# Kernel optimization log

Hardware: AMD Instinct MI355X
Metric: run time of the kernel (lower is better)

The kernel has to match this reference:

```python
import jax, jax.numpy as jnp
import numpy as np
from jax import lax

DEPTH, HEADS, DH, DIM, M, V, NUM_EMB, D_VQ = 6, 8, 64, 512, 256, 523, 512, 64


def _ln(x, g, b):
    mu = jnp.mean(x, -1, keepdims=True)
    var = jnp.var(x, -1, keepdims=True)
    return (x - mu) * lax.rsqrt(var + 1e-5) * g + b


def _softmax_kernel(data, proj, is_query):
    # FAVOR+ positive softmax features (performer-pytorch softmax_kernel)
    dn = data * (data.shape[-1] ** -0.25)
    dd = jnp.einsum('bhld,md->bhlm', dn, proj)
    diag = 0.5 * jnp.sum(dn * dn, axis=-1, keepdims=True)
    mx = jnp.max(dd, axis=-1, keepdims=True) if is_query else jnp.max(dd)
    return jnp.exp(dd - diag - lax.stop_gradient(mx)) * (proj.shape[0] ** -0.5) + 1e-4


def _causal_linear_attn(qp, kp, v):
    # out_t = qp_t . cumsum_t(kp v^T) / (qp_t . cumsum_t(kp))
    kc = jnp.cumsum(kp, axis=2)
    den = jnp.einsum('bhlm,bhlm->bhl', qp, kc)
    kv = jnp.cumsum(jnp.einsum('bhlm,bhld->bhlmd', kp, v), axis=2)
    return jnp.einsum('bhlm,bhlmd->bhld', qp, kv) / den[..., None]


def _vq_encode(_x, conv1_w, conv1_b, conv2_w, conv2_b, codebook):
    dn = ('NCDHW', 'OIDHW', 'NCDHW')
    h = lax.conv_general_dilated(_x, conv1_w, (2, 2, 2), [(1, 1)] * 3, dimension_numbers=dn)
    h = jax.nn.relu(h + conv1_b[None, :, None, None, None])
    h = lax.conv_general_dilated(h, conv2_w, (2, 2, 2), [(1, 1)] * 3, dimension_numbers=dn)
    h = h + conv2_b[None, :, None, None, None]                 # [N, D, 4,4,4]
    z = jnp.transpose(h, (0, 2, 3, 4, 1))                      # [N, 4,4,4, D]
    flat = z.reshape(-1, z.shape[-1])
    d2 = (jnp.sum(flat * flat, 1, keepdims=True)
          - 2.0 * flat @ codebook.T
          + jnp.sum(codebook * codebook, 1)[None, :])
    inds = jnp.argmin(d2, axis=1).astype(jnp.int32)
    return inds.reshape(z.shape[:4])                           # [N, 4,4,4]


def _performer_loss(seq, tok_emb, pos_emb, proj, ln1_g, ln1_b, wq, wk, wv, wo, bo,
                    ln2_g, ln2_b, ff1_w, ff1_b, ff2_w, ff2_b, lnf_g, lnf_b,
                    logits_w, logits_b):
    inp, tgt = seq[:, :-1], seq[:, 1:]
    b, L = inp.shape
    h = tok_emb[inp] + pos_emb[:L][None]
    split = lambda t: jnp.transpose(t.reshape(b, L, HEADS, DH), (0, 2, 1, 3))
    for l in range(DEPTH):
        x1 = _ln(h, ln1_g[l], ln1_b[l])
        q, k, v = split(x1 @ wq[l]), split(x1 @ wk[l]), split(x1 @ wv[l])
        qp = _softmax_kernel(q, proj[l], True)
        kp = _softmax_kernel(k, proj[l], False)
        o = _causal_linear_attn(qp, kp, v)
        o = jnp.transpose(o, (0, 2, 1, 3)).reshape(b, L, DIM)
        h = h + o @ wo[l] + bo[l]
        x2 = _ln(h, ln2_g[l], ln2_b[l])
        h = h + jax.nn.gelu(x2 @ ff1_w[l] + ff1_b[l]) @ ff2_w[l] + ff2_b[l]
    h = _ln(h, lnf_g, lnf_b)
    logits = h @ logits_w + logits_b
    lp = jax.nn.log_softmax(logits, axis=-1)
    nll = -jnp.take_along_axis(lp, tgt[..., None], axis=-1)[..., 0]
    return jnp.mean(nll)


def setup_inputs() -> dict:
    key = jax.random.key(0)
    ks = jax.random.split(key, 24)
    n = lambda k, sh, s=0.02: (jax.random.normal(k, sh) * s).astype(jnp.float32)
    bs = 16
    return {
        'x': jax.random.normal(ks[0], (bs, 1, 16, 16, 16), jnp.float32),
        'xn': jax.random.normal(ks[1], (bs, 1, 1, 16, 16, 16), jnp.float32),
        'i': jax.random.randint(ks[2], (bs, 3), 0, V, jnp.int32),
        # frozen VQ-VAE
        'conv1_w': n(ks[3], (32, 1, 4, 4, 4), 0.1), 'conv1_b': jnp.zeros((32,), jnp.float32),
        'conv2_w': n(ks[4], (D_VQ, 32, 4, 4, 4), 0.05), 'conv2_b': jnp.zeros((D_VQ,), jnp.float32),
        'codebook': jax.random.normal(ks[5], (NUM_EMB, D_VQ), jnp.float32),
        # FAVOR+ random-feature projections (non-trainable buffer)
        'proj': jax.random.normal(ks[6], (DEPTH, M, DH), jnp.float32),
        # performer params
        'tok_emb': n(ks[7], (V, DIM)), 'pos_emb': n(ks[8], (131, DIM)),
        'ln1_g': jnp.ones((DEPTH, DIM), jnp.float32), 'ln1_b': jnp.zeros((DEPTH, DIM), jnp.float32),
        'wq': n(ks[9], (DEPTH, DIM, DIM)), 'wk': n(ks[10], (DEPTH, DIM, DIM)),
        'wv': n(ks[11], (DEPTH, DIM, DIM)), 'wo': n(ks[12], (DEPTH, DIM, DIM)),
        'bo': jnp.zeros((DEPTH, DIM), jnp.float32),
        'ln2_g': jnp.ones((DEPTH, DIM), jnp.float32), 'ln2_b': jnp.zeros((DEPTH, DIM), jnp.float32),
        'ff1_w': n(ks[13], (DEPTH, DIM, 4 * DIM)), 'ff1_b': jnp.zeros((DEPTH, 4 * DIM), jnp.float32),
        'ff2_w': n(ks[14], (DEPTH, 4 * DIM, DIM)), 'ff2_b': jnp.zeros((DEPTH, DIM), jnp.float32),
        'lnf_g': jnp.ones((DIM,), jnp.float32), 'lnf_b': jnp.zeros((DIM,), jnp.float32),
        'logits_w': n(ks[15], (DIM, V)), 'logits_b': jnp.zeros((V,), jnp.float32),
    }


def reference(x, xn, i, conv1_w, conv1_b, conv2_w, conv2_b, codebook, proj,
              tok_emb, pos_emb, ln1_g, ln1_b, wq, wk, wv, wo, bo, ln2_g, ln2_b,
              ff1_w, ff1_b, ff2_w, ff2_b, lnf_g, lnf_b, logits_w, logits_b):
    bs = x.shape[0]
    _xn = xn.reshape((-1,) + xn.shape[2:])            # (b n) c x y z
    _x = jnp.concatenate([x, _xn], axis=0)
    inds = _vq_encode(_x, conv1_w, conv1_b, conv2_w, conv2_b, codebook)
    inds_i = inds[:bs].reshape(bs, -1)                # b (x y z)
    inds_r = inds[bs:].reshape(bs, -1)                # b (n x y z)
    seq = jnp.concatenate([i.astype(jnp.int32), inds_r, inds_i], axis=1)  # [b, 131]
    return _performer_loss(seq, tok_emb, pos_emb, proj, ln1_g, ln1_b, wq, wk, wv, wo,
                           bo, ln2_g, ln2_b, ff1_w, ff1_b, ff2_w, ff2_b,
                           lnf_g, lnf_b, logits_w, logits_b)
```

## Files before the change

### kernel.cpp

```cpp
#include <hip/hip_runtime.h>

#define SEQL 130
#define LSEQ 131
#define DIMM 512
#define NHEADS 8
#define MF 256
#define VSZ 523
#define NROWS (16*SEQL)
#define NBH (16*NHEADS)
#define NBHL (NBH*SEQL)
#define QSEG 1064960

typedef __attribute__((ext_vector_type(8))) short short8;
typedef __attribute__((ext_vector_type(8))) unsigned short us8;
typedef __attribute__((ext_vector_type(4))) unsigned short us4;
typedef __attribute__((ext_vector_type(4))) float f32x4;

__device__ __forceinline__ unsigned short f2bf(float f){
  unsigned int u = __float_as_uint(f);
  u += 0x7fffu + ((u>>16)&1u);
  return (unsigned short)(u>>16);
}
__device__ __forceinline__ float bf2f(unsigned short h){
  return __uint_as_float(((unsigned int)h)<<16);
}
__device__ __forceinline__ float gelu_f(float x){
  float x3 = x*x*x;
  return 0.5f*x*(1.f+tanhf(0.7978845608028654f*(x+0.044715f*x3)));
}
__device__ __forceinline__ unsigned enc_max(float f){
  unsigned u = __float_as_uint(f);
  return (u & 0x80000000u) ? ~u : (u | 0x80000000u);
}
__device__ __forceinline__ float dec_max(unsigned k){
  unsigned u = (k>>31) ? (k & 0x7fffffffu) : ~k;
  return __uint_as_float(u);
}
__device__ __forceinline__ float blk_sum(float v){
  #pragma unroll
  for(int off=32;off;off>>=1) v += __shfl_xor(v,off);
  __shared__ float tmp_s[4];
  int t=threadIdx.x;
  if((t&63)==0) tmp_s[t>>6]=v;
  __syncthreads();
  v = tmp_s[0]+tmp_s[1]+tmp_s[2]+tmp_s[3];
  __syncthreads();
  return v;
}
__device__ __forceinline__ float blk_max(float v){
  #pragma unroll
  for(int off=32;off;off>>=1) v = fmaxf(v,__shfl_xor(v,off));
  __shared__ float tmp_m[4];
  int t=threadIdx.x;
  if((t&63)==0) tmp_m[t>>6]=v;
  __syncthreads();
  v = fmaxf(fmaxf(tmp_m[0],tmp_m[1]),fmaxf(tmp_m[2],tmp_m[3]));
  __syncthreads();
  return v;
}

__global__ __launch_bounds__(256) void conv1_k(const float* __restrict__ x,
    const float* __restrict__ xn, const float* __restrict__ w,
    const float* __restrict__ bias, float* __restrict__ out){
  int idx = blockIdx.x*256 + threadIdx.x;
  if(idx >= 32*32*8*8*8) return;
  int ow = idx & 7, oh = (idx>>3)&7, od = (idx>>6)&7, oc = (idx>>9)&31, n = idx>>14;
  const float* xp = (n<16) ? (x + n*4096) : (xn + (n-16)*4096);
  const float* wp = w + oc*64;
  float acc = bias[oc];
  #pragma unroll
  for(int kd=0;kd<4;kd++){ int id = od*2-1+kd; if((unsigned)id>=16u) continue;
    #pragma unroll
    for(int kh=0;kh<4;kh++){ int ih = oh*2-1+kh; if((unsigned)ih>=16u) continue;
      #pragma unroll
      for(int kw=0;kw<4;kw++){ int iw = ow*2-1+kw; if((unsigned)iw>=16u) continue;
        acc += xp[(id*16+ih)*16+iw]*wp[(kd*4+kh)*4+kw];
      }}}
  out[idx] = fmaxf(acc,0.f);
}

__global__ __launch_bounds__(256) void conv2_k(const float* __restrict__ c1,
    const float* __restrict__ w, const float* __restrict__ bias,
    float* __restrict__ out){
  __shared__ float in_s[32][4][120];
  int od = blockIdx.x, n = blockIdx.y;
  int t = threadIdx.x;
  float4* zf = (float4*)&in_s[0][0][0];
  #pragma unroll
  for(int j=0;j<15;j++) zf[t + 256*j] = make_float4(0.f,0.f,0.f,0.f);
  __syncthreads();
  #pragma unroll
  for(int j=0;j<4;j++){
    int ridx = t + 256*j;
    int ic = ridx>>5, rem = ridx&31;
    int kd = rem>>3, ih = rem&7;
    int id = od*2 - 1 + kd;
    if((unsigned)id < 8u){
      const float* src = c1 + (size_t)(n*32+ic)*512 + id*64 + ih*8;
      float4 a = *(const float4*)src;
      float4 b = *(const float4*)(src+4);
      float* dst = &in_s[ic][kd][(ih+1)*12 + 1];
      dst[0]=a.x; dst[1]=a.y; dst[2]=a.z; dst[3]=a.w;
      dst[4]=b.x; dst[5]=b.y; dst[6]=b.z; dst[7]=b.w;
    }
  }
  __syncthreads();
  int oc = t>>2, oh = t&3;
  float acc0=bias[oc], acc1=acc0, acc2=acc0, acc3=acc0;
  for(int ic=0; ic<32; ic++){
    #pragma unroll
    for(int kd=0;kd<4;kd++){
      #pragma unroll
      for(int kh=0;kh<4;kh++){
        const float* rp = &in_s[ic][kd][(oh*2+kh)*12];
        f32x4 f0 = *(const f32x4*)rp;
        f32x4 f1 = *(const f32x4*)(rp+4);
        f32x4 f2 = *(const f32x4*)(rp+8);
        f32x4 wv = *(const f32x4*)(w + ((size_t)(oc*32+ic)*64 + (kd*4+kh)*4));
        float in0=f0[0],in1=f0[1],in2=f0[2],in3=f0[3];
        float in4=f1[0],in5=f1[1],in6=f1[2],in7=f1[3];
        float in8=f2[0],in9=f2[1];
        acc0 += wv[0]*in0 + wv[1]*in1 + wv[2]*in2 + wv[3]*in3;
        acc1 += wv[0]*in2 + wv[1]*in3 + wv[2]*in4 + wv[3]*in5;
        acc2 += wv[0]*in4 + wv[1]*in5 + wv[2]*in6 + wv[3]*in7;
        acc3 += wv[0]*in6 + wv[1]*in7 + wv[2]*in8 + wv[3]*in9;
      }
    }
  }
  float4 res = make_float4(acc0,acc1,acc2,acc3);
  *(float4*)(out + (size_t)(n*64+oc)*64 + od*16 + oh*4) = res;
}

__global__ __launch_bounds__(256) void vq_k(const float* __restrict__ c2,
    const float* __restrict__ cb, int* __restrict__ inds){
  int nf = blockIdx.x;
  int nb = nf>>6, sp = nf&63;
  __shared__ float z[64];
  int t = threadIdx.x;
  if(t<64) z[t] = c2[(nb*64+t)*64 + sp];
  __syncthreads();
  float best = 3.0e38f; int bi = 0;
  for(int j=t; j<512; j+=256){
    const float* cr = cb + j*64;
    float dot=0.f, nn=0.f;
    #pragma unroll 8
    for(int d=0;d<64;d++){ float cv=cr[d]; dot += z[d]*cv; nn += cv*cv; }
    float dist = nn - 2.f*dot;
    if(dist < best){ best=dist; bi=j; }
  }
  #pragma unroll
  for(int off=32;off;off>>=1){
    float ob = __shfl_down(best,off); int oi = __shfl_down(bi,off);
    if(ob<best || (ob==best && oi<bi)){ best=ob; bi=oi; }
  }
  __shared__ float rb[4]; __shared__ int ri[4];
  if((t&63)==0){ rb[t>>6]=best; ri[t>>6]=bi; }
  __syncthreads();
  if(t==0){
    for(int wv=1;wv<4;wv++){ if(rb[wv]<best || (rb[wv]==best && ri[wv]<bi)){ best=rb[wv]; bi=ri[wv]; } }
    inds[nf]=bi;
  }
}

__global__ void seq_k(const int* __restrict__ iarr, const int* __restrict__ inds,
                      int* __restrict__ seq){
  int idx = blockIdx.x*256 + threadIdx.x;
  if(idx >= 16*LSEQ) return;
  int b = idx/LSEQ, p = idx%LSEQ;
  int v;
  if(p<3)       v = iarr[b*3+p];
  else if(p<67) v = inds[(16+b)*64 + (p-3)];
  else          v = inds[b*64 + (p-67)];
  seq[idx] = v;
}

__global__ __launch_bounds__(256) void embed_k(const int* __restrict__ seq,
    const float* __restrict__ tok, const float* __restrict__ pos,
    float* __restrict__ h){
  int idx = blockIdx.x*256 + threadIdx.x;
  int c = idx & 511; int row = idx >> 9;
  int b = row/SEQL, l = row - b*SEQL;
  int tk = seq[b*LSEQ + l];
  h[idx] = tok[tk*DIMM + c] + pos[l*DIMM + c];
}

__global__ __launch_bounds__(256) void ln_k(const float* __restrict__ in,
    const float* __restrict__ g, const float* __restrict__ bb,
    unsigned short* __restrict__ out){
  int row = blockIdx.x; int t = threadIdx.x;
  const float* xr = in + (size_t)row*DIMM;
  float x0 = xr[t], x1 = xr[t+256];
  float s = x0+x1, ss = x0*x0 + x1*x1;
  #pragma unroll
  for(int off=32;off;off>>=1){ s += __shfl_xor(s,off); ss += __shfl_xor(ss,off); }
  __shared__ float bs[4], bss[4];
  if((t&63)==0){ bs[t>>6]=s; bss[t>>6]=ss; }
  __syncthreads();
  s = bs[0]+bs[1]+bs[2]+bs[3]; ss = bss[0]+bss[1]+bss[2]+bss[3];
  float mu = s*(1.f/512.f);
  float var = ss*(1.f/512.f) - mu*mu;
  float inv = rsqrtf(var + 1e-5f);
  out[(size_t)row*DIMM+t]     = f2bf((x0-mu)*inv*g[t]     + bb[t]);
  out[(size_t)row*DIMM+t+256] = f2bf((x1-mu)*inv*g[t+256] + bb[t+256]);
}

__global__ __launch_bounds__(256) void wprep_k(const float* __restrict__ wq_l,
    const float* __restrict__ wk_l, const float* __restrict__ wv_l,
    const float* __restrict__ wo_l, const float* __restrict__ ff1_l,
    const float* __restrict__ ff2_l,
    unsigned short* __restrict__ wqkvt, unsigned short* __restrict__ wot,
    unsigned short* __restrict__ ff1t, unsigned short* __restrict__ ff2t,
    unsigned int* __restrict__ gmaxbits){
  int bid = blockIdx.x;
  int t = threadIdx.x;
  if(bid==0 && t==0) gmaxbits[0] = 0u;
  const float* src; unsigned short* dst;
  int n0, k0, srcN, dstK;
  if(bid < 768){
    int nt = bid % 48, kt = bid / 48;
    n0 = nt*32; k0 = kt*32;
    int seg = n0 >> 9;
    src = (seg==0 ? wq_l : seg==1 ? wk_l : wv_l);
    dst = wqkvt; srcN = 512; dstK = 512;
    n0 &= 0x1ff; n0 |= (seg<<9);
  } else if(bid < 1024){
    int b2 = bid-768; int nt = b2 % 16, kt = b2 / 16;
    n0 = nt*32; k0 = kt*32; src = wo_l; dst = wot; srcN = 512; dstK = 512;
  } else if(bid < 2048){
    int b2 = bid-1024; int nt = b2 % 64, kt = b2 / 64;
    n0 = nt*32; k0 = kt*32; src = ff1_l; dst = ff1t; srcN = 2048; dstK = 512;
  } else {
    int b2 = bid-2048; int nt = b2 % 16, kt = b2 / 16;
    n0 = nt*32; k0 = kt*32; src = ff2_l; dst = ff2t; srcN = 512; dstK = 2048;
  }
  int srcCol0 = (bid < 768) ? (n0 & 0x1ff) : n0;
  __shared__ float tile[32][33];
  int c = t&31, r = t>>5;
  #pragma unroll
  for(int j=0;j<4;j++)
    tile[r+8*j][c] = src[(size_t)(k0+r+8*j)*srcN + srcCol0 + c];
  __syncthreads();
  #pragma unroll
  for(int j=0;j<4;j++){
    int n = n0 + r + 8*j;
    dst[(size_t)n*dstK + k0 + c] = f2bf(tile[c][r+8*j]);
  }
}

__global__ __launch_bounds__(256) void wconv_k(const float* __restrict__ W,
    unsigned short* __restrict__ dst, int K, int N){
  __shared__ float tile[32][33];
  int k0 = blockIdx.y*32, n0 = blockIdx.x*32;
  int t = threadIdx.x; int c = t&31, r = t>>5;
  #pragma unroll
  for(int j=0;j<4;j++){
    int n = n0+c;
    tile[r+8*j][c] = (n<N) ? W[(size_t)(k0+r+8*j)*N + n] : 0.f;
  }
  __syncthreads();
  #pragma unroll
  for(int j=0;j<4;j++){
    int n = n0 + r + 8*j;
    if(n<N) dst[(size_t)n*K + k0 + c] = f2bf(tile[c][r+8*j]);
  }
}

__global__ __launch_bounds__(256) void projcv_k(const float* __restrict__ proj,
    unsigned short* __restrict__ pb){
  int i = blockIdx.x*256 + threadIdx.x;
  if(i < 6*MF*64) pb[i] = f2bf(proj[i]);
}

template<int MODE>
__global__ __launch_bounds__(256) void mgemm_k(const unsigned short* __restrict__ A,
    const unsigned short* __restrict__ Bt, const float* __restrict__ bias,
    float* __restrict__ Cf, unsigned short* __restrict__ Cb,
    int M, int N, int K){
  __shared__ unsigned short As[4096];
  __shared__ unsigned short Bs[4096];
  int t = threadIdx.x;
  const int m0 = blockIdx.y*64, n0 = blockIdx.x*64;
  int w = t>>6, l = t&63;
  int wr = w>>1, wc = w&1;
  f32x4 acc[2][2] = {};
  int srow = t>>2, sp = (t&3)*2;
  int arow = m0 + srow, brow = n0 + srow;
  bool aok = arow < M, bok = brow < N;
  const us8* Ap = (const us8*)(A + (size_t)arow*K + sp*8);
  const us8* Bp = (const us8*)(Bt + (size_t)brow*K + sp*8);
  unsigned short* Aw0 = As + srow*64 + (((sp  )^(srow&7))<<3);
  unsigned short* Aw1 = As + srow*64 + (((sp+1)^(srow&7))<<3);
  unsigned short* Bw0 = Bs + srow*64 + (((sp  )^(srow&7))<<3);
  unsigned short* Bw1 = Bs + srow*64 + (((sp+1)^(srow&7))<<3);
  for(int k0=0; k0<K; k0+=64){
    us8 a0={}, a1={}, b0={}, b1={};
    if(aok){ a0 = Ap[0]; a1 = Ap[1]; }
    if(bok){ b0 = Bp[0]; b1 = Bp[1]; }
    Ap += 8; Bp += 8;
    __syncthreads();
    *(us8*)Aw0 = a0; *(us8*)Aw1 = a1;
    *(us8*)Bw0 = b0; *(us8*)Bw1 = b1;
    __syncthreads();
    #pragma unroll
    for(int kk=0;kk<2;kk++){
      short8 af[2], bf[2];
      #pragma unroll
      for(int m=0;m<2;m++){
        int row = wr*32 + m*16 + (l&15);
        int slot = kk*4 + (l>>4);
        af[m] = *(const short8*)(As + row*64 + ((slot^(row&7))<<3));
      }
      #pragma unroll
      for(int n=0;n<2;n++){
        int col = wc*32 + n*16 + (l&15);
        int slot = kk*4 + (l>>4);
        bf[n] = *(const short8*)(Bs + col*64 + ((slot^(col&7))<<3));
      }
      #pragma unroll
      for(int m=0;m<2;m++)
        #pragma unroll
        for(int n=0;n<2;n++)
          acc[m][n] = __builtin_amdgcn_mfma_f32_16x16x32_bf16(af[m], bf[n], acc[m][n], 0, 0, 0);
    }
  }
  #pragma unroll
  for(int m=0;m<2;m++){
    #pragma unroll
    for(int n=0;n<2;n++){
      int col = n0 + wc*32 + n*16 + (l&15);
      #pragma unroll
      for(int i=0;i<4;i++){
        int row = m0 + wr*32 + m*16 + (l>>4)*4 + i;
        if(row < M && col < N){
          float v = acc[m][n][i];
          if(MODE==0){
            if(bias) v += bias[col];
            Cf[(size_t)row*N+col] = v;
          } else if(MODE==1){
            v *= (col < 1024) ? 0.35355339059327378f : 1.0f;
            int seg = col>>9, d0 = col&511;
            int hh = d0>>6, d = d0&63;
            int bb = row/SEQL, ll = row - bb*SEQL;
            Cb[(size_t)seg*QSEG + (((size_t)(bb*NHEADS+hh))*SEQL + ll)*64 + d] = f2bf(v);
          } else if(MODE==3){
            v += bias[col];
            Cf[(size_t)row*N+col] += v;
          } else {
            v += bias[col];
            v = gelu_f(v);
            Cb[(size_t)row*N+col] = f2bf(v);
          }
        }
      }
    }
  }
}

__global__ __launch_bounds__(256) void featA_k(const unsigned short* __restrict__ qn,
    const unsigned short* __restrict__ kn, const unsigned short* __restrict__ projl,
    unsigned short* __restrict__ qp, unsigned int* __restrict__ gmaxbits){
  int z = blockIdx.y;
  const unsigned short* dn = z ? kn : qn;
  __shared__ float uni[32*264];
  __shared__ unsigned short dns[2048];
  unsigned short* ps = (unsigned short*)uni;
  int t = threadIdx.x;
  size_t R0 = (size_t)blockIdx.x*32;
  {
    int row = t>>3, sl = t&7;
    us8 u = *(const us8*)(dn + (R0+row)*64 + sl*8);
    *(us8*)(dns + row*64 + ((sl^(row&7))<<3)) = u;
  }
  #pragma unroll
  for(int j=0;j<8;j++){
    int ridx = t + 256*j;
    int row = ridx>>3, sl = ridx&7;
    us8 u = *(const us8*)(projl + row*64 + sl*8);
    *(us8*)(ps + row*64 + ((sl^(row&7))<<3)) = u;
  }
  __syncthreads();
  int w = t>>6, l = t&63;
  int rt = w&1, cb = (w>>1)*8;
  f32x4 acc[8] = {};
  #pragma unroll
  for(int kk=0;kk<2;kk++){
    int ar = rt*16 + (l&15);
    int slot = kk*4 + (l>>4);
    short8 a = *(const short8*)(dns + ar*64 + ((slot^(ar&7))<<3));
    #pragma unroll
    for(int ct=0;ct<8;ct++){
      int br = (cb+ct)*16 + (l&15);
      short8 b = *(const short8*)(ps + br*64 + ((slot^(br&7))<<3));
      acc[ct] = __builtin_amdgcn_mfma_f32_16x16x32_bf16(a, b, acc[ct], 0, 0, 0);
    }
  }
  __syncthreads();
  #pragma unroll
  for(int ct=0;ct<8;ct++){
    int col = (cb+ct)*16 + (l&15);
    #pragma unroll
    for(int i=0;i<4;i++){
      int row = rt*16 + (l>>4)*4 + i;
      uni[row*264 + col] = acc[ct][i];
    }
  }
  __syncthreads();
  int r = t>>3, sub = t&7;
  float* rowp = uni + r*264 + sub*32;
  f32x4 v[8];
  #pragma unroll
  for(int jj=0;jj<8;jj++) v[jj] = *(const f32x4*)(rowp + jj*4);
  float m = -3.0e38f;
  #pragma unroll
  for(int jj=0;jj<8;jj++)
    #pragma unroll
    for(int i=0;i<4;i++) m = fmaxf(m, v[jj][i]);
  m = fmaxf(m, __shfl_xor(m,1));
  m = fmaxf(m, __shfl_xor(m,2));
  m = fmaxf(m, __shfl_xor(m,4));
  if(z==0){
    us8 dvu = *(const us8*)(dns + r*64 + ((sub^(r&7))<<3));
    float s2 = 0.f;
    #pragma unroll
    for(int j=0;j<8;j++){ float xx = bf2f(dvu[j]); s2 += xx*xx; }
    s2 += __shfl_xor(s2,1); s2 += __shfl_xor(s2,2); s2 += __shfl_xor(s2,4);
    float ds = 0.5f*s2;
    unsigned short* op = qp + (R0+r)*256 + sub*32;
    #pragma unroll
    for(int jj=0;jj<8;jj++){
      us4 u4;
      #pragma unroll
      for(int i=0;i<4;i++) u4[i] = f2bf(expf(v[jj][i] - ds - m)*0.0625f + 1e-4f);
      *(us4*)(op + jj*4) = u4;
    }
  } else {
    float bm = m;
    bm = fmaxf(bm, __shfl_xor(bm,8));
    bm = fmaxf(bm, __shfl_xor(bm,16));
    bm = fmaxf(bm, __shfl_xor(bm,32));
    __shared__ float wm[4];
    if(l==0) wm[w] = bm;
    __syncthreads();
    if(t==0){
      float g = fmaxf(fmaxf(wm[0],wm[1]),fmaxf(wm[2],wm[3]));
      atomicMax(gmaxbits, enc_max(g));
    }
  }
}

__global__ __launch_bounds__(256) void featB_k(const unsigned short* __restrict__ kn,
    const unsigned short* __restrict__ projl, const unsigned int* __restrict__ gmaxbits,
    unsigned short* __restrict__ kp){
  __shared__ float uni[32*264];
  __shared__ unsigned short dns[2048];
  unsigned short* ps = (unsigned short*)uni;
  int t = threadIdx.x;
  size_t R0 = (size_t)blockIdx.x*32;
  {
    int row = t>>3, sl = t&7;
    us8 u = *(const us8*)(kn + (R0+row)*64 + sl*8);
    *(us8*)(dns + row*64 + ((sl^(row&7))<<3)) = u;
  }
  #pragma unroll
  for(int j=0;j<8;j++){
    int ridx = t + 256*j;
    int row = ridx>>3, sl = ridx&7;
    us8 u = *(const us8*)(projl + row*64 + sl*8);
    *(us8*)(ps + row*64 + ((sl^(row&7))<<3)) = u;
  }
  __syncthreads();
  int w = t>>6, l = t&63;
  int rt = w&1, cb = (w>>1)*8;
  f32x4 acc[8] = {};
  #pragma unroll
  for(int kk=0;kk<2;kk++){
    int ar = rt*16 + (l&15);
    int slot = kk*4 + (l>>4);
    short8 a = *(const short8*)(dns + ar*64 + ((slot^(ar&7))<<3));
    #pragma unroll
    for(int ct=0;ct<8;ct++){
      int br = (cb+ct)*16 + (l&15);
      short8 b = *(const short8*)(ps + br*64 + ((slot^(br&7))<<3));
      acc[ct] = __builtin_amdgcn_mfma_f32_16x16x32_bf16(a, b, acc[ct], 0, 0, 0);
    }
  }
  __syncthreads();
  #pragma unroll
  for(int ct=0;ct<8;ct++){
    int col = (cb+ct)*16 + (l&15);
    #pragma unroll
    for(int i=0;i<4;i++){
      int row = rt*16 + (l>>4)*4 + i;
      uni[row*264 + col] = acc[ct][i];
    }
  }
  __syncthreads();
  float g = dec_max(gmaxbits[0]);
  int r = t>>3, sub = t&7;
  us8 dvu = *(const us8*)(dns + r*64 + ((sub^(r&7))<<3));
  float s2 = 0.f;
  #pragma unroll
  for(int j=0;j<8;j++){ float xx = bf2f(dvu[j]); s2 += xx*xx; }
  s2 += __shfl_xor(s2,1); s2 += __shfl_xor(s2,2); s2 += __shfl_xor(s2,4);
  float ds = 0.5f*s2;
  float* rowp = uni + r*264 + sub*32;
  unsigned short* op = kp + (R0+r)*256 + sub*32;
  #pragma unroll
  for(int jj=0;jj<8;jj++){
    f32x4 v = *(const f32x4*)(rowp + jj*4);
    us4 u4;
    #pragma unroll
    for(int i=0;i<4;i++) u4[i] = f2bf(expf(v[i] - ds - g)*0.0625f + 1e-4f);
    *(us4*)(op + jj*4) = u4;
  }
}

__global__ __launch_bounds__(256) void attn_k(const unsigned short* __restrict__ qp,
    const unsigned short* __restrict__ kp, const unsigned short* __restrict__ vn,
    unsigned short* __restrict__ ob){
  int qt = blockIdx.x, bh = blockIdx.y;
  int b = bh>>3, hh = bh&7;
  __shared__ unsigned short qs[32*256];
  __shared__ unsigned short ks[32*256];
  __shared__ float vs[32][68];
  __shared__ float Ss[32][33];
  __shared__ float dens[2][32];
  int t = threadIdx.x;
  int w = t>>6, l = t&63;
  int qh = w>>1, kh = w&1;
  {
    int rr = t>>3, s0 = (t&7)*4;
    int gr = qt*32 + rr;
    const us8* src = (const us8*)(qp + ((size_t)bh*SEQL + (gr<SEQL?gr:0))*256 + s0*8);
    #pragma unroll
    for(int j=0;j<4;j++){
      us8 u = {};
      if(gr<SEQL) u = src[j];
      *(us8*)(qs + rr*256 + (((s0+j)^(rr&7))<<3)) = u;
    }
  }
  if(t<64) dens[t>>5][t&31] = 0.f;
  float o[8] = {0.f,0.f,0.f,0.f,0.f,0.f,0.f,0.f};
  int orow = t>>3, od = (t&7)*8;
  for(int kt=0; kt<=qt; kt++){
    __syncthreads();
    {
      int rr = t>>3, s0 = (t&7)*4;
      int gk = kt*32 + rr;
      const us8* src = (const us8*)(kp + ((size_t)bh*SEQL + (gk<SEQL?gk:0))*256 + s0*8);
      #pragma unroll
      for(int j=0;j<4;j++){
        us8 u = {};
        if(gk<SEQL) u = src[j];
        *(us8*)(ks + rr*256 + (((s0+j)^(rr&7))<<3)) = u;
      }
      const us8* vsrc = (const us8*)(vn + ((size_t)bh*SEQL + (gk<SEQL?gk:0))*64 + od);
      us8 uv = {};
      if(gk<SEQL) uv = vsrc[0];
      #pragma unroll
      for(int i=0;i<8;i++) vs[rr][od+i] = bf2f(uv[i]);
    }
    __syncthreads();
    f32x4 sacc = {};
    #pragma unroll
    for(int kk=0;kk<8;kk++){
      int ar = qh*16 + (l&15); int slot = kk*4 + (l>>4);
      short8 a = *(const short8*)(qs + ar*256 + ((slot^(ar&7))<<3));
      int br = kh*16 + (l&15);
      short8 bb2 = *(const short8*)(ks + br*256 + ((slot^(br&7))<<3));
      sacc = __builtin_amdgcn_mfma_f32_16x16x32_bf16(a, bb2, sacc, 0, 0, 0);
    }
    int scol = kh*16 + (l&15);
    int gcol = kt*32 + scol;
    float dp[4];
    #pragma unroll
    for(int i=0;i<4;i++){
      int sr = qh*16 + (l>>4)*4 + i;
      int grw = qt*32 + sr;
      float v2 = sacc[i];
      if(gcol > grw) v2 = 0.f;
      Ss[sr][scol] = v2;
      dp[i] = v2;
    }
    #pragma unroll
    for(int off=1;off<16;off<<=1)
      #pragma unroll
      for(int i=0;i<4;i++) dp[i] += __shfl_xor(dp[i], off);
    if((l&15)==0){
      #pragma unroll
      for(int i=0;i<4;i++) dens[kh][qh*16 + (l>>4)*4 + i] += dp[i];
    }
    __syncthreads();
    #pragma unroll
    for(int k2=0;k2<32;k2++){
      float s = Ss[orow][k2];
      #pragma unroll
      for(int j=0;j<8;j++) o[j] += s*vs[k2][od+j];
    }
  }
  __syncthreads();
  int gr = qt*32 + orow;
  if(gr < SEQL){
    float inv = 1.f/(dens[0][orow] + dens[1][orow]);
    us8 u;
    #pragma unroll
    for(int j=0;j<8;j++) u[j] = f2bf(o[j]*inv);
    *(us8*)(ob + ((size_t)(b*SEQL+gr))*DIMM + hh*64 + od) = u;
  }
}

__global__ __launch_bounds__(256) void loss_k(const float* __restrict__ logits,
    const int* __restrict__ seq, float* __restrict__ rnll){
  int row = blockIdx.x; int t = threadIdx.x;
  const float* lr = logits + (size_t)row*VSZ;
  float m = -3.0e38f;
  for(int j=t;j<VSZ;j+=256) m = fmaxf(m, lr[j]);
  m = blk_max(m);
  float s = 0.f;
  for(int j=t;j<VSZ;j+=256) s += expf(lr[j]-m);
  s = blk_sum(s);
  if(t==0){
    int b = row/SEQL, l = row - b*SEQL;
    int tgt = seq[b*LSEQ + l + 1];
    rnll[row] = (m + logf(s)) - lr[tgt];
  }
}

__global__ __launch_bounds__(256) void fin_k(const float* __restrict__ rnll,
    float* __restrict__ out){
  int t = threadIdx.x;
  float s = 0.f;
  for(int i=t;i<NROWS;i+=256) s += rnll[i];
  s = blk_sum(s);
  if(t==0) out[0] = s/(float)NROWS;
}

extern "C" void kernel_launch(void* const* d_in, const int* in_sizes, int n_in,
                              void* d_out, int out_size, void* d_ws, size_t ws_size,
                              hipStream_t stream){
  (void)in_sizes; (void)n_in; (void)out_size; (void)ws_size;
  const float* x        = (const float*)d_in[0];
  const float* xn       = (const float*)d_in[1];
  const int*   iarr     = (const int*)  d_in[2];
  const float* conv1_w  = (const float*)d_in[3];
  const float* conv1_b  = (const float*)d_in[4];
  const float* conv2_w  = (const float*)d_in[5];
  const float* conv2_b  = (const float*)d_in[6];
  const float* codebook = (const float*)d_in[7];
  const float* proj     = (const float*)d_in[8];
  const float* tok_emb  = (const float*)d_in[9];
  const float* pos_emb  = (const float*)d_in[10];
  const float* ln1_g    = (const float*)d_in[11];
  const float* ln1_b    = (const float*)d_in[12];
  const float* wq       = (const float*)d_in[13];
  const float* wk       = (const float*)d_in[14];
  const float* wv       = (const float*)d_in[15];
  const float* wo       = (const float*)d_in[16];
  const float* bo       = (const float*)d_in[17];
  const float* ln2_g    = (const float*)d_in[18];
  const float* ln2_b    = (const float*)d_in[19];
  const float* ff1_w    = (const float*)d_in[20];
  const float* ff1_b    = (const float*)d_in[21];
  const float* ff2_w    = (const float*)d_in[22];
  const float* ff2_b    = (const float*)d_in[23];
  const float* lnf_g    = (const float*)d_in[24];
  const float* lnf_b    = (const float*)d_in[25];
  const float* logits_w = (const float*)d_in[26];
  const float* logits_b = (const float*)d_in[27];

  float* wsf = (float*)d_ws;
  size_t off = 0;
  unsigned short* qp_bf = (unsigned short*)(wsf + off); off += 2129920;
  unsigned short* kp_bf = (unsigned short*)(wsf + off); off += 2129920;
  float* h = wsf + off; off += 1064960;
  unsigned short* x1b = (unsigned short*)(wsf + off); off += 532480;
  unsigned short* qkvb = (unsigned short*)(wsf + off); off += 1597440;
  unsigned short* ob  = (unsigned short*)(wsf + off); off += 532480;
  unsigned short* projb = (unsigned short*)(wsf + off); off += 49152;
  unsigned short* wqkvt = (unsigned short*)(wsf + off); off += 393216;
  unsigned short* wot   = (unsigned short*)(wsf + off); off += 131072;
  unsigned short* ff1t  = (unsigned short*)(wsf + off); off += 524288;
  unsigned short* ff2t  = (unsigned short*)(wsf + off); off += 524288;
  unsigned short* logt  = (unsigned short*)(wsf + off); off += 133888;
  unsigned short* ffmid = (unsigned short*)(wsf + off); off += 2129920;
  float* logits = wsf + off; off += 1087840;
  int* inds = (int*)(wsf + off); off += 2048;
  int* seq  = (int*)(wsf + off); off += 2112;
  unsigned int* gmaxbits = (unsigned int*)(wsf + off); off += 64;
  float* rnll = wsf + off; off += 2112;

  float* c1 = (float*)ffmid;
  float* c2 = ((float*)ffmid) + 524288;

  unsigned short* qnb = qkvb;
  unsigned short* knb = qkvb + QSEG;
  unsigned short* vnb = qkvb + 2*QSEG;

  conv1_k<<<2048,256,0,stream>>>(x, xn, conv1_w, conv1_b, c1);
  conv2_k<<<dim3(4,32),256,0,stream>>>(c1, conv2_w, conv2_b, c2);
  vq_k<<<2048,256,0,stream>>>(c2, codebook, inds);
  seq_k<<<(16*LSEQ+255)/256,256,0,stream>>>(iarr, inds, seq);
  embed_k<<<(NROWS*DIMM)/256,256,0,stream>>>(seq, tok_emb, pos_emb, h);
  projcv_k<<<384,256,0,stream>>>(proj, projb);
  wconv_k<<<dim3(17,16),256,0,stream>>>(logits_w, logt, 512, 523);

  for(int l=0;l<6;l++){
    wprep_k<<<3072,256,0,stream>>>(wq + (size_t)l*262144, wk + (size_t)l*262144,
        wv + (size_t)l*262144, wo + (size_t)l*262144,
        ff1_w + (size_t)l*1048576, ff2_w + (size_t)l*1048576,
        wqkvt, wot, ff1t, ff2t, gmaxbits);
    ln_k<<<NROWS,256,0,stream>>>(h, ln1_g+l*DIMM, ln1_b+l*DIMM, x1b);
    mgemm_k<1><<<dim3(24,33),256,0,stream>>>(x1b, wqkvt, nullptr, nullptr, qkvb, NROWS, 1536, DIMM);
    featA_k<<<dim3(520,2),256,0,stream>>>(qnb, knb, projb + l*16384, qp_bf, gmaxbits);
    featB_k<<<520,256,0,stream>>>(knb, projb + l*16384, gmaxbits, kp_bf);
    attn_k<<<dim3(5,NBH),256,0,stream>>>(qp_bf, kp_bf, vnb, ob);
    mgemm_k<3><<<dim3(8,33),256,0,stream>>>(ob, wot, bo+l*DIMM, h, nullptr, NROWS, DIMM, DIMM);
    ln_k<<<NROWS,256,0,stream>>>(h, ln2_g+l*DIMM, ln2_b+l*DIMM, x1b);
    mgemm_k<4><<<dim3(32,33),256,0,stream>>>(x1b, ff1t, ff1_b+l*2048, nullptr, ffmid, NROWS, 2048, DIMM);
    mgemm_k<3><<<dim3(8,33),256,0,stream>>>(ffmid, ff2t, ff2_b+l*DIMM, h, nullptr, NROWS, DIMM, 2048);
  }

  ln_k<<<NROWS,256,0,stream>>>(h, lnf_g, lnf_b, x1b);
  mgemm_k<0><<<dim3(9,33),256,0,stream>>>(x1b, logt, logits_b, logits, nullptr, NROWS, VSZ, DIMM);
  loss_k<<<NROWS,256,0,stream>>>(logits, seq, rnll);
  fin_k<<<1,256,0,stream>>>(rnll, (float*)d_out);
}
```

Before: 852.1 us.

## Add 32-row MFMA GEMM for residual projections, split conv2, drop seq kernel

The out-projection and FF2 residual GEMMs (N=512) now use a new kernel with 32x64 tiles, launching 520 blocks instead of 264 to fill more compute units. conv2 is split over two output-channel groups with 512 threads each computing one output, which raises parallelism but loses the register reuse of computing four outputs per thread. The seq_k kernel is removed and tokens are gathered inline in embed and loss. A redundant index remap in wprep is also dropped. The new GEMM has no double buffering, and smaller tiles re-read the A operand more often.

Measured after the change: 796.0 us. 1.07x faster.

```diff
diff --git a/kernel.cpp b/kernel.cpp
--- a/kernel.cpp
+++ b/kernel.cpp
@@ -58,6 +58,12 @@
   __syncthreads();
   return v;
 }
+__device__ __forceinline__ int tok_at(const int* __restrict__ iarr,
+    const int* __restrict__ inds, int b, int p){
+  if(p<3)  return iarr[b*3+p];
+  if(p<67) return inds[(16+b)*64 + (p-3)];
+  return inds[b*64 + (p-67)];
+}
 
 __global__ __launch_bounds__(256) void conv1_k(const float* __restrict__ x,
     const float* __restrict__ xn, const float* __restrict__ w,
@@ -79,19 +85,22 @@
   out[idx] = fmaxf(acc,0.f);
 }
 
-__global__ __launch_bounds__(256) void conv2_k(const float* __restrict__ c1,
+__global__ __launch_bounds__(512) void conv2_k(const float* __restrict__ c1,
     const float* __restrict__ w, const float* __restrict__ bias,
     float* __restrict__ out){
   __shared__ float in_s[32][4][120];
-  int od = blockIdx.x, n = blockIdx.y;
+  int od = blockIdx.x, n = blockIdx.y, ocg = blockIdx.z;
   int t = threadIdx.x;
   float4* zf = (float4*)&in_s[0][0][0];
   #pragma unroll
-  for(int j=0;j<15;j++) zf[t + 256*j] = make_float4(0.f,0.f,0.f,0.f);
-  __syncthreads();
-  #pragma unroll
-  for(int j=0;j<4;j++){
-    int ridx = t + 256*j;
+  for(int j=0;j<8;j++){
+    int idx = t + 512*j;
+    if(idx < 3840) zf[idx] = make_float4(0.f,0.f,0.f,0.f);
+  }
+  __syncthreads();
+  #pragma unroll
+  for(int j=0;j<2;j++){
+    int ridx = t + 512*j;
     int ic = ridx>>5, rem = ridx&31;
     int kd = rem>>3, ih = rem&7;
     int id = od*2 - 1 + kd;
@@ -105,30 +114,21 @@
     }
   }
   __syncthreads();
-  int oc = t>>2, oh = t&3;
-  float acc0=bias[oc], acc1=acc0, acc2=acc0, acc3=acc0;
+  int oc = ocg*32 + (t>>4);
+  int oh = (t>>2)&3, ow = t&3;
+  float acc = bias[oc];
   for(int ic=0; ic<32; ic++){
     #pragma unroll
     for(int kd=0;kd<4;kd++){
       #pragma unroll
       for(int kh=0;kh<4;kh++){
-        const float* rp = &in_s[ic][kd][(oh*2+kh)*12];
-        f32x4 f0 = *(const f32x4*)rp;
-        f32x4 f1 = *(const f32x4*)(rp+4);
-        f32x4 f2 = *(const f32x4*)(rp+8);
         f32x4 wv = *(const f32x4*)(w + ((size_t)(oc*32+ic)*64 + (kd*4+kh)*4));
-        float in0=f0[0],in1=f0[1],in2=f0[2],in3=f0[3];
-        float in4=f1[0],in5=f1[1],in6=f1[2],in7=f1[3];
-        float in8=f2[0],in9=f2[1];
-        acc0 += wv[0]*in0 + wv[1]*in1 + wv[2]*in2 + wv[3]*in3;
-        acc1 += wv[0]*in2 + wv[1]*in3 + wv[2]*in4 + wv[3]*in5;
-        acc2 += wv[0]*in4 + wv[1]*in5 + wv[2]*in6 + wv[3]*in7;
-        acc3 += wv[0]*in6 + wv[1]*in7 + wv[2]*in8 + wv[3]*in9;
+        const float* base = &in_s[ic][kd][(oh*2+kh)*12 + ow*2];
+        acc += wv[0]*base[0] + wv[1]*base[1] + wv[2]*base[2] + wv[3]*base[3];
       }
     }
   }
-  float4 res = make_float4(acc0,acc1,acc2,acc3);
-  *(float4*)(out + (size_t)(n*64+oc)*64 + od*16 + oh*4) = res;
+  out[(size_t)(n*64+oc)*64 + od*16 + oh*4 + ow] = acc;
 }
 
 __global__ __launch_bounds__(256) void vq_k(const float* __restrict__ c2,
@@ -162,25 +162,13 @@
   }
 }
 
-__global__ void seq_k(const int* __restrict__ iarr, const int* __restrict__ inds,
-                      int* __restrict__ seq){
-  int idx = blockIdx.x*256 + threadIdx.x;
-  if(idx >= 16*LSEQ) return;
-  int b = idx/LSEQ, p = idx%LSEQ;
-  int v;
-  if(p<3)       v = iarr[b*3+p];
-  else if(p<67) v = inds[(16+b)*64 + (p-3)];
-  else          v = inds[b*64 + (p-67)];
-  seq[idx] = v;
-}
-
-__global__ __launch_bounds__(256) void embed_k(const int* __restrict__ seq,
-    const float* __restrict__ tok, const float* __restrict__ pos,
-    float* __restrict__ h){
+__global__ __launch_bounds__(256) void embed_k(const int* __restrict__ iarr,
+    const int* __restrict__ inds, const float* __restrict__ tok,
+    const float* __restrict__ pos, float* __restrict__ h){
   int idx = blockIdx.x*256 + threadIdx.x;
   int c = idx & 511; int row = idx >> 9;
   int b = row/SEQL, l = row - b*SEQL;
-  int tk = seq[b*LSEQ + l];
+  int tk = tok_at(iarr, inds, b, l);
   h[idx] = tok[tk*DIMM + c] + pos[l*DIMM + c];
 }
 
@@ -222,7 +210,6 @@
     int seg = n0 >> 9;
     src = (seg==0 ? wq_l : seg==1 ? wk_l : wv_l);
     dst = wqkvt; srcN = 512; dstK = 512;
-    n0 &= 0x1ff; n0 |= (seg<<9);
   } else if(bid < 1024){
     int b2 = bid-768; int nt = b2 % 16, kt = b2 / 16;
     n0 = nt*32; k0 = kt*32; src = wo_l; dst = wot; srcN = 512; dstK = 512;
@@ -356,6 +343,56 @@
   }
 }
 
+__global__ __launch_bounds__(256) void mgemm32_k(const unsigned short* __restrict__ A,
+    const unsigned short* __restrict__ Bt, const float* __restrict__ bias,
+    float* __restrict__ Cf, int N, int K){
+  __shared__ unsigned short As[2048];
+  __shared__ unsigned short Bs[4096];
+  int t = threadIdx.x;
+  const int m0 = blockIdx.y*32, n0 = blockIdx.x*64;
+  int w = t>>6, l = t&63;
+  int wm = w&1, wn2 = w>>1;
+  f32x4 acc[2] = {};
+  int srowA = t>>3, spA = t&7;
+  int srowB = t>>2, spB = (t&3)*2;
+  const us8* Ap = (const us8*)(A + (size_t)(m0+srowA)*K + spA*8);
+  const us8* Bp = (const us8*)(Bt + (size_t)(n0+srowB)*K + spB*8);
+  unsigned short* Aw  = As + srowA*64 + ((spA^(srowA&7))<<3);
+  unsigned short* Bw0 = Bs + srowB*64 + (((spB  )^(srowB&7))<<3);
+  unsigned short* Bw1 = Bs + srowB*64 + (((spB+1)^(srowB&7))<<3);
+  for(int k0=0; k0<K; k0+=64){
+    us8 a0 = Ap[0];
+    us8 b0 = Bp[0], b1 = Bp[1];
+    Ap += 8; Bp += 8;
+    __syncthreads();
+    *(us8*)Aw = a0;
+    *(us8*)Bw0 = b0; *(us8*)Bw1 = b1;
+    __syncthreads();
+    #pragma unroll
+    for(int kk=0;kk<2;kk++){
+      int arow = wm*16 + (l&15);
+      int slot = kk*4 + (l>>4);
+      short8 af = *(const short8*)(As + arow*64 + ((slot^(arow&7))<<3));
+      #pragma unroll
+      for(int n=0;n<2;n++){
+        int col = (wn2*2+n)*16 + (l&15);
+        short8 bf = *(const short8*)(Bs + col*64 + ((slot^(col&7))<<3));
+        acc[n] = __builtin_amdgcn_mfma_f32_16x16x32_bf16(af, bf, acc[n], 0, 0, 0);
+      }
+    }
+  }
+  #pragma unroll
+  for(int n=0;n<2;n++){
+    int col = n0 + (wn2*2+n)*16 + (l&15);
+    float bv = bias[col];
+    #pragma unroll
+    for(int i=0;i<4;i++){
+      int row = m0 + wm*16 + (l>>4)*4 + i;
+      Cf[(size_t)row*N+col] += acc[n][i] + bv;
+    }
+  }
+}
+
 __global__ __launch_bounds__(256) void featA_k(const unsigned short* __restrict__ qn,
     const unsigned short* __restrict__ kn, const unsigned short* __restrict__ projl,
     unsigned short* __restrict__ qp, unsigned int* __restrict__ gmaxbits){
@@ -610,7 +647,8 @@
 }
 
 __global__ __launch_bounds__(256) void loss_k(const float* __restrict__ logits,
-    const int* __restrict__ seq, float* __restrict__ rnll){
+    const int* __restrict__ iarr, const int* __restrict__ inds,
+    float* __restrict__ rnll){
   int row = blockIdx.x; int t = threadIdx.x;
   const float* lr = logits + (size_t)row*VSZ;
   float m = -3.0e38f;
@@ -621,7 +659,7 @@
   s = blk_sum(s);
   if(t==0){
     int b = row/SEQL, l = row - b*SEQL;
-    int tgt = seq[b*LSEQ + l + 1];
+    int tgt = tok_at(iarr, inds, b, l+1);
     rnll[row] = (m + logf(s)) - lr[tgt];
   }
 }
@@ -685,7 +723,6 @@
   unsigned short* ffmid = (unsigned short*)(wsf + off); off += 2129920;
   float* logits = wsf + off; off += 1087840;
   int* inds = (int*)(wsf + off); off += 2048;
-  int* seq  = (int*)(wsf + off); off += 2112;
   unsigned int* gmaxbits = (unsigned int*)(wsf + off); off += 64;
   float* rnll = wsf + off; off += 2112;
 
@@ -697,10 +734,9 @@
   unsigned short* vnb = qkvb + 2*QSEG;
 
   conv1_k<<<2048,256,0,stream>>>(x, xn, conv1_w, conv1_b, c1);
-  conv2_k<<<dim3(4,32),256,0,stream>>>(c1, conv2_w, conv2_b, c2);
+  conv2_k<<<dim3(4,32,2),512,0,stream>>>(c1, conv2_w, conv2_b, c2);
   vq_k<<<2048,256,0,stream>>>(c2, codebook, inds);
-  seq_k<<<(16*LSEQ+255)/256,256,0,stream>>>(iarr, inds, seq);
-  embed_k<<<(NROWS*DIMM)/256,256,0,stream>>>(seq, tok_emb, pos_emb, h);
+  embed_k<<<(NROWS*DIMM)/256,256,0,stream>>>(iarr, inds, tok_emb, pos_emb, h);
   projcv_k<<<384,256,0,stream>>>(proj, projb);
   wconv_k<<<dim3(17,16),256,0,stream>>>(logits_w, logt, 512, 523);
 
@@ -714,14 +750,14 @@
     featA_k<<<dim3(520,2),256,0,stream>>>(qnb, knb, projb + l*16384, qp_bf, gmaxbits);
     featB_k<<<520,256,0,stream>>>(knb, projb + l*16384, gmaxbits, kp_bf);
     attn_k<<<dim3(5,NBH),256,0,stream>>>(qp_bf, kp_bf, vnb, ob);
-    mgemm_k<3><<<dim3(8,33),256,0,stream>>>(ob, wot, bo+l*DIMM, h, nullptr, NROWS, DIMM, DIMM);
+    mgemm32_k<<<dim3(8,65),256,0,stream>>>(ob, wot, bo+l*DIMM, h, DIMM, DIMM);
     ln_k<<<NROWS,256,0,stream>>>(h, ln2_g+l*DIMM, ln2_b+l*DIMM, x1b);
     mgemm_k<4><<<dim3(32,33),256,0,stream>>>(x1b, ff1t, ff1_b+l*2048, nullptr, ffmid, NROWS, 2048, DIMM);
-    mgemm_k<3><<<dim3(8,33),256,0,stream>>>(ffmid, ff2t, ff2_b+l*DIMM, h, nullptr, NROWS, DIMM, 2048);
+    mgemm32_k<<<dim3(8,65),256,0,stream>>>(ffmid, ff2t, ff2_b+l*DIMM, h, DIMM, 2048);
   }
 
   ln_k<<<NROWS,256,0,stream>>>(h, lnf_g, lnf_b, x1b);
   mgemm_k<0><<<dim3(9,33),256,0,stream>>>(x1b, logt, logits_b, logits, nullptr, NROWS, VSZ, DIMM);
-  loss_k<<<NROWS,256,0,stream>>>(logits, seq, rnll);
+  loss_k<<<NROWS,256,0,stream>>>(logits, iarr, inds, rnll);
   fin_k<<<1,256,0,stream>>>(rnll, (float*)d_out);
 }
```
